# Performance work log

Measured on AMD Instinct MI355X. Metric: run time of the kernel, lower is better.

The kernel has to match this reference:

```python
import jax, jax.numpy as jnp
import numpy as np

B, T, D, H = 4, 2048, 1024, 16
HD = D // H  # head dim = 64


def setup_inputs() -> dict:
    key = jax.random.key(0)
    ks = jax.random.split(key, 12)
    s = 1.0 / np.sqrt(D)
    inp = {
        "Q": jax.random.normal(ks[0], (B, T, D), jnp.float32),
        "K": jax.random.normal(ks[1], (B, T, D), jnp.float32),
        "V": jax.random.normal(ks[2], (B, T, D), jnp.float32),
        "mask": jnp.tril(jnp.ones((T, T), jnp.int32))[None, None],  # causal [1,1,T,T]
        "Wq": jax.random.normal(ks[3], (D, D), jnp.float32) * s,
        "bq": jax.random.normal(ks[4], (D,), jnp.float32) * s,
        "Wk": jax.random.normal(ks[5], (D, D), jnp.float32) * s,
        "bk": jax.random.normal(ks[6], (D,), jnp.float32) * s,
        "Wv": jax.random.normal(ks[7], (D, D), jnp.float32) * s,
        "bv": jax.random.normal(ks[8], (D,), jnp.float32) * s,
        "Wo": jax.random.normal(ks[9], (D, D), jnp.float32) * s,
        "bo": jax.random.normal(ks[10], (D,), jnp.float32) * s,
    }
    return inp


def reference(Q, K, V, mask, Wq, bq, Wk, bk, Wv, bv, Wo, bo):
    b, t, d = Q.shape
    # projections (torch Linear: x @ W^T + b)
    q = (Q @ Wq.T + bq).reshape(b, t, H, HD).transpose(0, 2, 1, 3)  # [b,h,t,hd]
    k = (K @ Wk.T + bk).reshape(b, t, H, HD).transpose(0, 2, 1, 3)
    v = (V @ Wv.T + bv).reshape(b, t, H, HD).transpose(0, 2, 1, 3)
    score = jnp.einsum("bhqd,bhkd->bhqk", q, k) / jnp.sqrt(jnp.float32(HD))
    score = jnp.where(mask == 0, jnp.float32(-1e9), score)
    attn = jax.nn.softmax(score, axis=-1)
    out = jnp.einsum("bhqk,bhkd->bhqd", attn, v)
    out = out.transpose(0, 2, 1, 3).reshape(b, t, d)
    return out @ Wo.T + bo
```

## Files before the change

### kernel.cpp

```cpp
#include <hip/hip_runtime.h>
#include <stdint.h>

#define B_SZ  4
#define T_SEQ 2048
#define DIM   1024
#define NH    16
#define HD    64
#define M_TOT (B_SZ * T_SEQ)

typedef unsigned short u16;
typedef unsigned long long u64;
typedef __attribute__((ext_vector_type(8))) __bf16 bf16x8;
typedef __attribute__((ext_vector_type(4))) float  floatx4;
typedef __attribute__((ext_vector_type(16))) float floatx16;

#define SCL_Q (0.125f * 1.44269504089f)

__device__ __forceinline__ u16 f2bf(float f) {
  union { float f; uint32_t u; } v; v.f = f;
  uint32_t r = v.u + 0x7fffu + ((v.u >> 16) & 1u);
  return (u16)(r >> 16);
}

__device__ __forceinline__ void gl_lds16(const void* g, void* l) {
  __builtin_amdgcn_global_load_lds(
      (const __attribute__((address_space(1))) uint32_t*)g,
      (__attribute__((address_space(3))) uint32_t*)l, 16, 0, 0);
}

__global__ __launch_bounds__(256) void cvt_all(
    const float* __restrict__ s0, const float* __restrict__ s1,
    const float* __restrict__ s2, const float* __restrict__ s3,
    const float* __restrict__ s4, const float* __restrict__ s5,
    const float* __restrict__ s6,
    u16* __restrict__ d0, u16* __restrict__ d1, u16* __restrict__ d2,
    u16* __restrict__ d3, u16* __restrict__ d4, u16* __restrict__ d5,
    u16* __restrict__ d6) {
  const float* s; u16* d; int n;
  switch (blockIdx.y) {
    case 0: s = s0; d = d0; n = DIM * DIM; break;
    case 1: s = s1; d = d1; n = DIM * DIM; break;
    case 2: s = s2; d = d2; n = DIM * DIM; break;
    case 3: s = s3; d = d3; n = DIM * DIM; break;
    case 4: s = s4; d = d4; n = M_TOT * DIM; break;
    case 5: s = s5; d = d5; n = M_TOT * DIM; break;
    default: s = s6; d = d6; n = M_TOT * DIM; break;
  }
  int i = (blockIdx.x * 256 + threadIdx.x) * 8;
  if (i >= n) return;
  float4 a = *(const float4*)(s + i);
  float4 b = *(const float4*)(s + i + 4);
  uint4 o;
  o.x = (uint32_t)f2bf(a.x) | ((uint32_t)f2bf(a.y) << 16);
  o.y = (uint32_t)f2bf(a.z) | ((uint32_t)f2bf(a.w) << 16);
  o.z = (uint32_t)f2bf(b.x) | ((uint32_t)f2bf(b.y) << 16);
  o.w = (uint32_t)f2bf(b.z) | ((uint32_t)f2bf(b.w) << 16);
  *(uint4*)(d + i) = o;
}

#define BKG 64
__global__ __launch_bounds__(256) void gemm_qkv(
    const u16* __restrict__ Qb, const u16* __restrict__ Kb,
    const u16* __restrict__ Vb,
    const u16* __restrict__ Wq, const u16* __restrict__ Wk,
    const u16* __restrict__ Wv,
    const float* __restrict__ bq, const float* __restrict__ bk,
    const float* __restrict__ bv,
    u16* __restrict__ qo, u16* __restrict__ ko, u16* __restrict__ vo) {
  const u16* A; const u16* Bw; const float* bias; u16* Co;
  if (blockIdx.z == 0)      { A = Qb; Bw = Wq; bias = bq; Co = qo; }
  else if (blockIdx.z == 1) { A = Kb; Bw = Wk; bias = bk; Co = ko; }
  else                      { A = Vb; Bw = Wv; bias = bv; Co = vo; }

  __shared__ u16 As[128 * 64];
  __shared__ u16 Bs[128 * 64];

  const int tid  = threadIdx.x;
  const int wave = tid >> 6, lane = tid & 63;
  const int quad = lane >> 4, l16 = lane & 15;
  const int wm = wave >> 1, wn = wave & 1;
  const int m0 = blockIdx.x * 128, n0 = blockIdx.y * 128;

  const floatx4 FZ = {0.f, 0.f, 0.f, 0.f};
  floatx4 acc[4][4];
#pragma unroll
  for (int mt = 0; mt < 4; ++mt)
#pragma unroll
    for (int nt = 0; nt < 4; ++nt) acc[mt][nt] = FZ;

  for (int k0 = 0; k0 < DIM; k0 += BKG) {
    __syncthreads();
#pragma unroll
    for (int j = 0; j < 4; ++j) {
      int pc = j * 256 + tid;
      int r = pc >> 3, c = pc & 7;
      int sc = c ^ (r & 7);
      gl_lds16(A  + (size_t)(m0 + r) * DIM + k0 + sc * 8,
               &As[(j * 256 + wave * 64) * 8]);
      gl_lds16(Bw + (size_t)(n0 + r) * DIM + k0 + sc * 8,
               &Bs[(j * 256 + wave * 64) * 8]);
    }
    __syncthreads();

#pragma unroll
    for (int kk = 0; kk < 2; ++kk) {
      bf16x8 af[4], bfr[4];
#pragma unroll
      for (int mt = 0; mt < 4; ++mt) {
        int ra = wm * 64 + mt * 16 + l16;
        af[mt] = *(const bf16x8*)&As[ra * 64 + (((kk * 4 + quad) ^ (ra & 7)) * 8)];
      }
#pragma unroll
      for (int nt = 0; nt < 4; ++nt) {
        int rb = wn * 64 + nt * 16 + l16;
        bfr[nt] = *(const bf16x8*)&Bs[rb * 64 + (((kk * 4 + quad) ^ (rb & 7)) * 8)];
      }
#pragma unroll
      for (int mt = 0; mt < 4; ++mt)
#pragma unroll
        for (int nt = 0; nt < 4; ++nt)
          acc[mt][nt] = __builtin_amdgcn_mfma_f32_16x16x32_bf16(
              af[mt], bfr[nt], acc[mt][nt], 0, 0, 0);
    }
  }

  if (blockIdx.z == 2) {
#pragma unroll
    for (int nt = 0; nt < 4; ++nt) {
      int n = n0 + wn * 64 + nt * 16 + l16;
      float bb = bias[n];
      int h = n >> 6, hd = n & 63;
#pragma unroll
      for (int mt = 0; mt < 4; ++mt) {
        int mbase = m0 + wm * 64 + mt * 16 + quad * 4;
        int b = mbase >> 11, t = mbase & (T_SEQ - 1);
        u64 pk = 0;
#pragma unroll
        for (int r = 0; r < 4; ++r)
          pk |= (u64)f2bf(acc[mt][nt][r] + bb) << (16 * r);
        *(u64*)&Co[((size_t)((b * NH + h) * HD + hd)) * T_SEQ + t] = pk;
      }
    }
  } else {
    const float sc = (blockIdx.z == 0) ? SCL_Q : 1.0f;
#pragma unroll
    for (int nt = 0; nt < 4; ++nt) {
      int n = n0 + wn * 64 + nt * 16 + l16;
      float bb = bias[n];
      int h = n >> 6, hd = n & 63;
#pragma unroll
      for (int mt = 0; mt < 4; ++mt) {
#pragma unroll
        for (int r = 0; r < 4; ++r) {
          int m = m0 + wm * 64 + mt * 16 + quad * 4 + r;
          int b = m >> 11, t = m & (T_SEQ - 1);
          Co[((size_t)(b * NH + h) * T_SEQ + t) * HD + hd] =
              f2bf((acc[mt][nt][r] + bb) * sc);
        }
      }
    }
  }
}

__global__ __launch_bounds__(256, 2) void flash_attn(
    const u16* __restrict__ qp, const u16* __restrict__ kp,
    const u16* __restrict__ vp, u16* __restrict__ ao) {
  const int bh = blockIdx.x;
  const int y = blockIdx.y;
  const int qt = (y < 4) ? (7 - y) : (y - 4);
  const int b = bh >> 4, h = bh & 15;
  const u16* Qg = qp + (size_t)bh * T_SEQ * HD;
  const u16* Kg = kp + (size_t)bh * T_SEQ * HD;
  const u16* Vg = vp + (size_t)bh * HD * T_SEQ;

  __shared__ u16 lds[6][64 * 64];

  const int tid = threadIdx.x, wave = tid >> 6, lane = tid & 63;
  const int hi = lane >> 5, c31 = lane & 31;
  const int lr8 = lane >> 3, lc8 = lane & 7;

  const int wbase = qt * 256 + wave * 64;
  const int qrowA = wbase + c31;
  const int qrowB = qrowA + 32;

  bf16x8 bqA[4], bqB[4];
#pragma unroll
  for (int cth = 0; cth < 4; ++cth) {
    bqA[cth] = *(const bf16x8*)(Qg + (size_t)qrowA * HD + cth * 16 + hi * 8);
    bqB[cth] = *(const bf16x8*)(Qg + (size_t)qrowB * HD + cth * 16 + hi * 8);
  }

  const int nkb = 4 * qt + 4;

#define STAGE_KV(kbidx, bufpair)                                              \
  {                                                                           \
    const u16* Kgk = Kg + (size_t)(kbidx) * 64 * HD;                          \
    const u16* Vgk = Vg + (size_t)(kbidx) * 64;                               \
    _Pragma("unroll") for (int i_ = 0; i_ < 2; ++i_) {                        \
      int r_ = i_ * 32 + wave * 8 + lr8;                                      \
      int sc_ = lc8 ^ (r_ & 7);                                               \
      gl_lds16(Kgk + (size_t)r_ * HD + sc_ * 8,                               \
               &lds[(bufpair) * 2][(i_ * 32 + wave * 8) * 64]);               \
      gl_lds16(Vgk + (size_t)r_ * T_SEQ + sc_ * 8,                            \
               &lds[(bufpair) * 2 + 1][(i_ * 32 + wave * 8) * 64]);           \
    }                                                                         \
  }

  STAGE_KV(0, 0);
  STAGE_KV(1, 1);

  asm volatile("" :: "v"(bqA[0]), "v"(bqA[1]), "v"(bqA[2]), "v"(bqA[3]),
                     "v"(bqB[0]), "v"(bqB[1]), "v"(bqB[2]), "v"(bqB[3]));

  floatx16 oA0, oA1, oB0, oB1;
#pragma unroll
  for (int i = 0; i < 16; ++i) { oA0[i] = 0.f; oA1[i] = 0.f;
                                 oB0[i] = 0.f; oB1[i] = 0.f; }
  float l_pA = 0.f, l_pB = 0.f;

  int koff[4];
#pragma unroll
  for (int x = 0; x < 4; ++x)
    koff[x] = c31 * 64 + (((x * 2 + hi) ^ (c31 & 7)) * 8);

  int pcb = 0;
  int psb = 2;
  for (int kb = 0; kb < nkb; ++kb) {
    if (kb + 1 < nkb) asm volatile("s_waitcnt vmcnt(4)" ::: "memory");
    else              asm volatile("s_waitcnt vmcnt(0)" ::: "memory");
    __builtin_amdgcn_s_barrier();
    __builtin_amdgcn_sched_barrier(0);

    if (kb + 2 < nkb) {
      STAGE_KV(kb + 2, psb);
      psb = (psb == 2) ? 0 : psb + 1;
    }

    if (kb * 64 <= wbase + 63) {
      const u16* Ks = &lds[pcb * 2][0];
      const u16* Vs = &lds[pcb * 2 + 1][0];

      floatx16 sA0, sA1, sB0, sB1;
#pragma unroll
      for (int i = 0; i < 16; ++i) { sA0[i] = 0.f; sA1[i] = 0.f;
                                     sB0[i] = 0.f; sB1[i] = 0.f; }
#pragma unroll
      for (int cth = 0; cth < 4; ++cth) {
        bf16x8 ka = *(const bf16x8*)&Ks[koff[cth]];
        bf16x8 kh = *(const bf16x8*)&Ks[koff[cth] + 32 * 64];
        sA0 = __builtin_amdgcn_mfma_f32_32x32x16_bf16(ka, bqA[cth], sA0, 0, 0, 0);
        sA1 = __builtin_amdgcn_mfma_f32_32x32x16_bf16(kh, bqA[cth], sA1, 0, 0, 0);
        sB0 = __builtin_amdgcn_mfma_f32_32x32x16_bf16(ka, bqB[cth], sB0, 0, 0, 0);
        sB1 = __builtin_amdgcn_mfma_f32_32x32x16_bf16(kh, bqB[cth], sB1, 0, 0, 0);
      }

      if (kb * 64 + 63 > wbase) {
        int kvb = kb * 64 + 4 * hi;
#pragma unroll
        for (int r = 0; r < 16; ++r) {
          int kvr = kvb + (r & 3) + 8 * (r >> 2);
          if (kvr > qrowA)      sA0[r] = -3e38f;
          if (kvr + 32 > qrowA) sA1[r] = -3e38f;
          if (kvr > qrowB)      sB0[r] = -3e38f;
          if (kvr + 32 > qrowB) sB1[r] = -3e38f;
        }
      }

      uint32_t pkA0[8], pkA1[8], pkB0[8], pkB1[8];
      float rsA = 0.f, rsB = 0.f;
#pragma unroll
      for (int rr = 0; rr < 8; ++rr) {
        union { float f; uint32_t u; } x0, x1, y0, y1;
        x0.f = __builtin_amdgcn_exp2f(sA0[2 * rr]);
        x1.f = __builtin_amdgcn_exp2f(sA0[2 * rr + 1]);
        y0.f = __builtin_amdgcn_exp2f(sA1[2 * rr]);
        y1.f = __builtin_amdgcn_exp2f(sA1[2 * rr + 1]);
        rsA += (x0.f + x1.f) + (y0.f + y1.f);
        pkA0[rr] = __builtin_amdgcn_perm(x1.u, x0.u, 0x07060302);
        pkA1[rr] = __builtin_amdgcn_perm(y1.u, y0.u, 0x07060302);
        x0.f = __builtin_amdgcn_exp2f(sB0[2 * rr]);
        x1.f = __builtin_amdgcn_exp2f(sB0[2 * rr + 1]);
        y0.f = __builtin_amdgcn_exp2f(sB1[2 * rr]);
        y1.f = __builtin_amdgcn_exp2f(sB1[2 * rr + 1]);
        rsB += (x0.f + x1.f) + (y0.f + y1.f);
        pkB0[rr] = __builtin_amdgcn_perm(x1.u, x0.u, 0x07060302);
        pkB1[rr] = __builtin_amdgcn_perm(y1.u, y0.u, 0x07060302);
      }
      l_pA += rsA;
      l_pB += rsB;

#pragma unroll
      for (int cc = 0; cc < 4; ++cc) {
        const uint32_t* pA = (cc & 2) ? pkA1 : pkA0;
        const uint32_t* pB = (cc & 2) ? pkB1 : pkB0;
        const int e4 = (cc & 1) * 4;
        auto a0 = __builtin_amdgcn_permlane32_swap(pA[e4 + 0], pA[e4 + 2],
                                                   false, false);
        auto a1 = __builtin_amdgcn_permlane32_swap(pA[e4 + 1], pA[e4 + 3],
                                                   false, false);
        auto b0 = __builtin_amdgcn_permlane32_swap(pB[e4 + 0], pB[e4 + 2],
                                                   false, false);
        auto b1 = __builtin_amdgcn_permlane32_swap(pB[e4 + 1], pB[e4 + 3],
                                                   false, false);
        union { uint32_t u[4]; bf16x8 v; } bpA, bpB;
        bpA.u[0] = a0[0]; bpA.u[1] = a1[0]; bpA.u[2] = a0[1]; bpA.u[3] = a1[1];
        bpB.u[0] = b0[0]; bpB.u[1] = b1[0]; bpB.u[2] = b0[1]; bpB.u[3] = b1[1];
        bf16x8 va = *(const bf16x8*)&Vs[koff[cc]];
        bf16x8 vb = *(const bf16x8*)&Vs[koff[cc] + 32 * 64];
        oA0 = __builtin_amdgcn_mfma_f32_32x32x16_bf16(va, bpA.v, oA0, 0, 0, 0);
        oA1 = __builtin_amdgcn_mfma_f32_32x32x16_bf16(vb, bpA.v, oA1, 0, 0, 0);
        oB0 = __builtin_amdgcn_mfma_f32_32x32x16_bf16(va, bpB.v, oB0, 0, 0, 0);
        oB1 = __builtin_amdgcn_mfma_f32_32x32x16_bf16(vb, bpB.v, oB1, 0, 0, 0);
      }
    }
    pcb = (pcb == 2) ? 0 : pcb + 1;
  }
#undef STAGE_KV

  {
    float lA = l_pA + __shfl_xor(l_pA, 32);
    float lB = l_pB + __shfl_xor(l_pB, 32);
    float invA = 1.0f / lA, invB = 1.0f / lB;
    const size_t obaseA = (size_t)(b * T_SEQ + qrowA) * DIM + h * HD;
    const size_t obaseB = obaseA + (size_t)32 * DIM;
#pragma unroll
    for (int u4 = 0; u4 < 4; ++u4) {
      u64 wA0 = 0, wA1 = 0, wB0 = 0, wB1 = 0;
#pragma unroll
      for (int r = 0; r < 4; ++r) {
        wA0 |= (u64)f2bf(oA0[4 * u4 + r] * invA) << (16 * r);
        wA1 |= (u64)f2bf(oA1[4 * u4 + r] * invA) << (16 * r);
        wB0 |= (u64)f2bf(oB0[4 * u4 + r] * invB) << (16 * r);
        wB1 |= (u64)f2bf(oB1[4 * u4 + r] * invB) << (16 * r);
      }
      *(u64*)&ao[obaseA + 8 * u4 + 4 * hi] = wA0;
      *(u64*)&ao[obaseA + 32 + 8 * u4 + 4 * hi] = wA1;
      *(u64*)&ao[obaseB + 8 * u4 + 4 * hi] = wB0;
      *(u64*)&ao[obaseB + 32 + 8 * u4 + 4 * hi] = wB1;
    }
  }
}

__global__ __launch_bounds__(256) void gemm_out(
    const u16* __restrict__ Ain, const u16* __restrict__ Wo,
    const float* __restrict__ bo, float* __restrict__ out) {
  __shared__ u16 As[128 * 64];
  __shared__ u16 Bs[128 * 64];

  const int tid  = threadIdx.x;
  const int wave = tid >> 6, lane = tid & 63;
  const int quad = lane >> 4, l16 = lane & 15;
  const int wm = wave >> 1, wn = wave & 1;
  const int m0 = blockIdx.x * 128, n0 = blockIdx.y * 128;

  const floatx4 FZ = {0.f, 0.f, 0.f, 0.f};
  floatx4 acc[4][4];
#pragma unroll
  for (int mt = 0; mt < 4; ++mt)
#pragma unroll
    for (int nt = 0; nt < 4; ++nt) acc[mt][nt] = FZ;

  for (int k0 = 0; k0 < DIM; k0 += BKG) {
    __syncthreads();
#pragma unroll
    for (int j = 0; j < 4; ++j) {
      int pc = j * 256 + tid;
      int r = pc >> 3, c = pc & 7;
      int sc = c ^ (r & 7);
      gl_lds16(Ain + (size_t)(m0 + r) * DIM + k0 + sc * 8,
               &As[(j * 256 + wave * 64) * 8]);
      gl_lds16(Wo  + (size_t)(n0 + r) * DIM + k0 + sc * 8,
               &Bs[(j * 256 + wave * 64) * 8]);
    }
    __syncthreads();

#pragma unroll
    for (int kk = 0; kk < 2; ++kk) {
      bf16x8 af[4], bfr[4];
#pragma unroll
      for (int mt = 0; mt < 4; ++mt) {
        int ra = wm * 64 + mt * 16 + l16;
        af[mt] = *(const bf16x8*)&As[ra * 64 + (((kk * 4 + quad) ^ (ra & 7)) * 8)];
      }
#pragma unroll
      for (int nt = 0; nt < 4; ++nt) {
        int rb = wn * 64 + nt * 16 + l16;
        bfr[nt] = *(const bf16x8*)&Bs[rb * 64 + (((kk * 4 + quad) ^ (rb & 7)) * 8)];
      }
#pragma unroll
      for (int mt = 0; mt < 4; ++mt)
#pragma unroll
        for (int nt = 0; nt < 4; ++nt)
          acc[mt][nt] = __builtin_amdgcn_mfma_f32_16x16x32_bf16(
              af[mt], bfr[nt], acc[mt][nt], 0, 0, 0);
    }
  }

#pragma unroll
  for (int nt = 0; nt < 4; ++nt) {
    int n = n0 + wn * 64 + nt * 16 + l16;
    float bb = bo[n];
#pragma unroll
    for (int mt = 0; mt < 4; ++mt)
#pragma unroll
      for (int r = 0; r < 4; ++r) {
        int m = m0 + wm * 64 + mt * 16 + quad * 4 + r;
        out[(size_t)m * DIM + n] = acc[mt][nt][r] + bb;
      }
  }
}

extern "C" void kernel_launch(void* const* d_in, const int* in_sizes, int n_in,
                              void* d_out, int out_size, void* d_ws,
                              size_t ws_size, hipStream_t stream) {
  const float* Q  = (const float*)d_in[0];
  const float* K  = (const float*)d_in[1];
  const float* V  = (const float*)d_in[2];
  const float* Wq = (const float*)d_in[4];
  const float* bq = (const float*)d_in[5];
  const float* Wk = (const float*)d_in[6];
  const float* bk = (const float*)d_in[7];
  const float* Wv = (const float*)d_in[8];
  const float* bv = (const float*)d_in[9];
  const float* Wo = (const float*)d_in[10];
  const float* bo = (const float*)d_in[11];
  float* out = (float*)d_out;

  u16* wqb = (u16*)d_ws;
  u16* wkb = wqb + 1048576;
  u16* wvb = wkb + 1048576;
  u16* wob = wvb + 1048576;
  u16* Qb  = wob + 1048576;
  u16* Kb  = Qb + (size_t)M_TOT * DIM;
  u16* Vb  = Kb + (size_t)M_TOT * DIM;
  u16* qp  = Vb + (size_t)M_TOT * DIM;
  u16* kp  = qp + (size_t)M_TOT * DIM;
  u16* vp  = kp + (size_t)M_TOT * DIM;
  u16* aop = vp + (size_t)M_TOT * DIM;

  cvt_all<<<dim3(M_TOT * DIM / 2048, 7), 256, 0, stream>>>(
      Wq, Wk, Wv, Wo, Q, K, V, wqb, wkb, wvb, wob, Qb, Kb, Vb);

  gemm_qkv<<<dim3(M_TOT / 128, DIM / 128, 3), 256, 0, stream>>>(
      Qb, Kb, Vb, wqb, wkb, wvb, bq, bk, bv, qp, kp, vp);

  flash_attn<<<dim3(B_SZ * NH, T_SEQ / 256), 256, 0, stream>>>(qp, kp, vp, aop);

  gemm_out<<<dim3(M_TOT / 128, DIM / 128), 256, 0, stream>>>(aop, wob, bo, out);
}
```

Measured before the change: 308.2 us.

## Fuse fp32-to-bf16 activation conversion into QKV GEMM and double-buffer weights

Drops the separate conversion pass over the Q/K/V activations. The QKV GEMM now reads fp32 rows straight from global memory into registers and converts them to bf16 just before the MFMA, so the bf16 activation copies no longer have to be written and read back. The weight tile is double-buffered in LDS with async global-to-LDS loads for the next k-step. The cost is that each block re-reads A rows from global memory as fp32, at twice the bytes, across the 8 column blocks of the grid, with no LDS sharing. These loads are per-lane 16-byte reads with a stride of one row, which may coalesce poorly.

New measurement: 427.0 us. 38.6% more time.

```diff
diff --git a/kernel.cpp b/kernel.cpp
--- a/kernel.cpp
+++ b/kernel.cpp
@@ -28,26 +28,19 @@
       (__attribute__((address_space(3))) uint32_t*)l, 16, 0, 0);
 }
 
-__global__ __launch_bounds__(256) void cvt_all(
+__global__ __launch_bounds__(256) void cvt_w(
     const float* __restrict__ s0, const float* __restrict__ s1,
     const float* __restrict__ s2, const float* __restrict__ s3,
-    const float* __restrict__ s4, const float* __restrict__ s5,
-    const float* __restrict__ s6,
     u16* __restrict__ d0, u16* __restrict__ d1, u16* __restrict__ d2,
-    u16* __restrict__ d3, u16* __restrict__ d4, u16* __restrict__ d5,
-    u16* __restrict__ d6) {
-  const float* s; u16* d; int n;
+    u16* __restrict__ d3) {
+  const float* s; u16* d;
   switch (blockIdx.y) {
-    case 0: s = s0; d = d0; n = DIM * DIM; break;
-    case 1: s = s1; d = d1; n = DIM * DIM; break;
-    case 2: s = s2; d = d2; n = DIM * DIM; break;
-    case 3: s = s3; d = d3; n = DIM * DIM; break;
-    case 4: s = s4; d = d4; n = M_TOT * DIM; break;
-    case 5: s = s5; d = d5; n = M_TOT * DIM; break;
-    default: s = s6; d = d6; n = M_TOT * DIM; break;
+    case 0: s = s0; d = d0; break;
+    case 1: s = s1; d = d1; break;
+    case 2: s = s2; d = d2; break;
+    default: s = s3; d = d3; break;
   }
   int i = (blockIdx.x * 256 + threadIdx.x) * 8;
-  if (i >= n) return;
   float4 a = *(const float4*)(s + i);
   float4 b = *(const float4*)(s + i + 4);
   uint4 o;
@@ -58,22 +51,22 @@
   *(uint4*)(d + i) = o;
 }
 
-#define BKG 64
+#define BKG  64
+#define NT_K (DIM / BKG)
 __global__ __launch_bounds__(256) void gemm_qkv(
-    const u16* __restrict__ Qb, const u16* __restrict__ Kb,
-    const u16* __restrict__ Vb,
+    const float* __restrict__ Qf, const float* __restrict__ Kf,
+    const float* __restrict__ Vf,
     const u16* __restrict__ Wq, const u16* __restrict__ Wk,
     const u16* __restrict__ Wv,
     const float* __restrict__ bq, const float* __restrict__ bk,
     const float* __restrict__ bv,
     u16* __restrict__ qo, u16* __restrict__ ko, u16* __restrict__ vo) {
-  const u16* A; const u16* Bw; const float* bias; u16* Co;
-  if (blockIdx.z == 0)      { A = Qb; Bw = Wq; bias = bq; Co = qo; }
-  else if (blockIdx.z == 1) { A = Kb; Bw = Wk; bias = bk; Co = ko; }
-  else                      { A = Vb; Bw = Wv; bias = bv; Co = vo; }
-
-  __shared__ u16 As[128 * 64];
-  __shared__ u16 Bs[128 * 64];
+  const float* A; const u16* Bw; const float* bias; u16* Co;
+  if (blockIdx.z == 0)      { A = Qf; Bw = Wq; bias = bq; Co = qo; }
+  else if (blockIdx.z == 1) { A = Kf; Bw = Wk; bias = bk; Co = ko; }
+  else                      { A = Vf; Bw = Wv; bias = bv; Co = vo; }
+
+  __shared__ u16 Bs[2][128 * 64];
 
   const int tid  = threadIdx.x;
   const int wave = tid >> 6, lane = tid & 63;
@@ -88,41 +81,66 @@
 #pragma unroll
     for (int nt = 0; nt < 4; ++nt) acc[mt][nt] = FZ;
 
-  for (int k0 = 0; k0 < DIM; k0 += BKG) {
-    __syncthreads();
-#pragma unroll
-    for (int j = 0; j < 4; ++j) {
-      int pc = j * 256 + tid;
-      int r = pc >> 3, c = pc & 7;
-      int sc = c ^ (r & 7);
-      gl_lds16(A  + (size_t)(m0 + r) * DIM + k0 + sc * 8,
-               &As[(j * 256 + wave * 64) * 8]);
-      gl_lds16(Bw + (size_t)(n0 + r) * DIM + k0 + sc * 8,
-               &Bs[(j * 256 + wave * 64) * 8]);
-    }
-    __syncthreads();
+  const float* arow0 = A + (size_t)(m0 + wm * 64 + 0 * 16 + l16) * DIM + quad * 8;
+  const float* arow1 = A + (size_t)(m0 + wm * 64 + 1 * 16 + l16) * DIM + quad * 8;
+  const float* arow2 = A + (size_t)(m0 + wm * 64 + 2 * 16 + l16) * DIM + quad * 8;
+  const float* arow3 = A + (size_t)(m0 + wm * 64 + 3 * 16 + l16) * DIM + quad * 8;
+
+#define STAGE_B(kt)                                                           \
+  { _Pragma("unroll") for (int j_ = 0; j_ < 4; ++j_) {                        \
+      int pc_ = j_ * 256 + tid; int r_ = pc_ >> 3, c_ = pc_ & 7;              \
+      int sc_ = c_ ^ (r_ & 7);                                                \
+      gl_lds16(Bw + (size_t)(n0 + r_) * DIM + (kt) * BKG + sc_ * 8,           \
+               &Bs[(kt) & 1][(j_ * 256 + wave * 64) * 8]); } }
+
+  STAGE_B(0);
+  __syncthreads();
+
+  for (int t = 0; t < NT_K; ++t) {
+    const int k0 = t * BKG;
+
+    float4 a4[4][2][2];
+#pragma unroll
+    for (int kk = 0; kk < 2; ++kk)
+#pragma unroll
+      for (int h = 0; h < 2; ++h) {
+        a4[0][kk][h] = *(const float4*)(arow0 + k0 + kk * 32 + h * 4);
+        a4[1][kk][h] = *(const float4*)(arow1 + k0 + kk * 32 + h * 4);
+        a4[2][kk][h] = *(const float4*)(arow2 + k0 + kk * 32 + h * 4);
+        a4[3][kk][h] = *(const float4*)(arow3 + k0 + kk * 32 + h * 4);
+      }
+
+    if (t + 1 < NT_K) STAGE_B(t + 1);
+
+    bf16x8 bfr[4][2];
+#pragma unroll
+    for (int nt = 0; nt < 4; ++nt) {
+      int rb = wn * 64 + nt * 16 + l16;
+#pragma unroll
+      for (int kk = 0; kk < 2; ++kk)
+        bfr[nt][kk] = *(const bf16x8*)
+            &Bs[t & 1][rb * 64 + (((kk * 4 + quad) ^ (rb & 7)) * 8)];
+    }
 
 #pragma unroll
     for (int kk = 0; kk < 2; ++kk) {
-      bf16x8 af[4], bfr[4];
 #pragma unroll
       for (int mt = 0; mt < 4; ++mt) {
-        int ra = wm * 64 + mt * 16 + l16;
-        af[mt] = *(const bf16x8*)&As[ra * 64 + (((kk * 4 + quad) ^ (ra & 7)) * 8)];
-      }
-#pragma unroll
-      for (int nt = 0; nt < 4; ++nt) {
-        int rb = wn * 64 + nt * 16 + l16;
-        bfr[nt] = *(const bf16x8*)&Bs[rb * 64 + (((kk * 4 + quad) ^ (rb & 7)) * 8)];
-      }
-#pragma unroll
-      for (int mt = 0; mt < 4; ++mt)
+        float4 lo = a4[mt][kk][0], hi = a4[mt][kk][1];
+        bf16x8 af;
+        af[0] = (__bf16)lo.x; af[1] = (__bf16)lo.y;
+        af[2] = (__bf16)lo.z; af[3] = (__bf16)lo.w;
+        af[4] = (__bf16)hi.x; af[5] = (__bf16)hi.y;
+        af[6] = (__bf16)hi.z; af[7] = (__bf16)hi.w;
 #pragma unroll
         for (int nt = 0; nt < 4; ++nt)
           acc[mt][nt] = __builtin_amdgcn_mfma_f32_16x16x32_bf16(
-              af[mt], bfr[nt], acc[mt][nt], 0, 0, 0);
-    }
-  }
+              af, bfr[nt][kk], acc[mt][nt], 0, 0, 0);
+      }
+    }
+    __syncthreads();
+  }
+#undef STAGE_B
 
   if (blockIdx.z == 2) {
 #pragma unroll
@@ -430,19 +448,16 @@
   u16* wkb = wqb + 1048576;
   u16* wvb = wkb + 1048576;
   u16* wob = wvb + 1048576;
-  u16* Qb  = wob + 1048576;
-  u16* Kb  = Qb + (size_t)M_TOT * DIM;
-  u16* Vb  = Kb + (size_t)M_TOT * DIM;
-  u16* qp  = Vb + (size_t)M_TOT * DIM;
+  u16* qp  = wob + 1048576;
   u16* kp  = qp + (size_t)M_TOT * DIM;
   u16* vp  = kp + (size_t)M_TOT * DIM;
   u16* aop = vp + (size_t)M_TOT * DIM;
 
-  cvt_all<<<dim3(M_TOT * DIM / 2048, 7), 256, 0, stream>>>(
-      Wq, Wk, Wv, Wo, Q, K, V, wqb, wkb, wvb, wob, Qb, Kb, Vb);
+  cvt_w<<<dim3(DIM * DIM / 2048, 4), 256, 0, stream>>>(
+      Wq, Wk, Wv, Wo, wqb, wkb, wvb, wob);
 
   gemm_qkv<<<dim3(M_TOT / 128, DIM / 128, 3), 256, 0, stream>>>(
-      Qb, Kb, Vb, wqb, wkb, wvb, bq, bk, bv, qp, kp, vp);
+      Q, K, V, wqb, wkb, wvb, bq, bk, bv, qp, kp, vp);
 
   flash_attn<<<dim3(B_SZ * NH, T_SEQ / 256), 256, 0, stream>>>(qp, kp, vp, aop);
 
```

## Triple-buffer QKV projection GEMM with async global-to-LDS prefetch

Applied to the files above, without the earlier changes.

Reworks the QKV projection GEMM main loop into a three-stage LDS ring buffer with K-tile 32. Loads for tile t+2 are issued before computing tile t, and each iteration uses a single barrier guarded by explicit vmcnt waits instead of two syncthreads. The goal is to hide global load latency behind MFMA work. The cost is more loop iterations with less compute each, a new XOR swizzle for 32-wide rows, and hand-managed waitcnt correctness. The output-projection GEMM keeps a hardcoded K step of 64.

Measured after the change: 318.3 us. 1.03x slower.

```diff
diff --git a/kernel.cpp b/kernel.cpp
--- a/kernel.cpp
+++ b/kernel.cpp
@@ -58,7 +58,8 @@
   *(uint4*)(d + i) = o;
 }
 
-#define BKG 64
+#define BKG  32
+#define NT_K (DIM / BKG)
 __global__ __launch_bounds__(256) void gemm_qkv(
     const u16* __restrict__ Qb, const u16* __restrict__ Kb,
     const u16* __restrict__ Vb,
@@ -72,12 +73,13 @@
   else if (blockIdx.z == 1) { A = Kb; Bw = Wk; bias = bk; Co = ko; }
   else                      { A = Vb; Bw = Wv; bias = bv; Co = vo; }
 
-  __shared__ u16 As[128 * 64];
-  __shared__ u16 Bs[128 * 64];
+  __shared__ u16 As[3][128 * 32];
+  __shared__ u16 Bs[3][128 * 32];
 
   const int tid  = threadIdx.x;
   const int wave = tid >> 6, lane = tid & 63;
   const int quad = lane >> 4, l16 = lane & 15;
+  const int lr4 = lane >> 2, lc4 = lane & 3;
   const int wm = wave >> 1, wn = wave & 1;
   const int m0 = blockIdx.x * 128, n0 = blockIdx.y * 128;
 
@@ -88,41 +90,55 @@
 #pragma unroll
     for (int nt = 0; nt < 4; ++nt) acc[mt][nt] = FZ;
 
-  for (int k0 = 0; k0 < DIM; k0 += BKG) {
-    __syncthreads();
-#pragma unroll
-    for (int j = 0; j < 4; ++j) {
-      int pc = j * 256 + tid;
-      int r = pc >> 3, c = pc & 7;
-      int sc = c ^ (r & 7);
-      gl_lds16(A  + (size_t)(m0 + r) * DIM + k0 + sc * 8,
-               &As[(j * 256 + wave * 64) * 8]);
-      gl_lds16(Bw + (size_t)(n0 + r) * DIM + k0 + sc * 8,
-               &Bs[(j * 256 + wave * 64) * 8]);
-    }
-    __syncthreads();
-
-#pragma unroll
-    for (int kk = 0; kk < 2; ++kk) {
-      bf16x8 af[4], bfr[4];
-#pragma unroll
-      for (int mt = 0; mt < 4; ++mt) {
-        int ra = wm * 64 + mt * 16 + l16;
-        af[mt] = *(const bf16x8*)&As[ra * 64 + (((kk * 4 + quad) ^ (ra & 7)) * 8)];
-      }
-#pragma unroll
-      for (int nt = 0; nt < 4; ++nt) {
-        int rb = wn * 64 + nt * 16 + l16;
-        bfr[nt] = *(const bf16x8*)&Bs[rb * 64 + (((kk * 4 + quad) ^ (rb & 7)) * 8)];
-      }
-#pragma unroll
-      for (int mt = 0; mt < 4; ++mt)
-#pragma unroll
-        for (int nt = 0; nt < 4; ++nt)
-          acc[mt][nt] = __builtin_amdgcn_mfma_f32_16x16x32_bf16(
-              af[mt], bfr[nt], acc[mt][nt], 0, 0, 0);
-    }
-  }
+#define STAGE_AB(kt, buf)                                                     \
+  { _Pragma("unroll") for (int i_ = 0; i_ < 2; ++i_) {                        \
+      int rb_ = wave * 32 + i_ * 16;                                          \
+      int r_ = rb_ + lr4;                                                     \
+      int sc_ = lc4 ^ ((r_ >> 1) & 3);                                        \
+      gl_lds16(A  + (size_t)(m0 + r_) * DIM + (kt) * BKG + sc_ * 8,           \
+               &As[buf][rb_ * 32]);                                           \
+      gl_lds16(Bw + (size_t)(n0 + r_) * DIM + (kt) * BKG + sc_ * 8,           \
+               &Bs[buf][rb_ * 32]);                                           \
+    } }
+
+  STAGE_AB(0, 0);
+  STAGE_AB(1, 1);
+
+  int rd = 0, st = 2;
+  for (int t = 0; t < NT_K; ++t) {
+    if (t + 1 < NT_K) asm volatile("s_waitcnt vmcnt(4)" ::: "memory");
+    else              asm volatile("s_waitcnt vmcnt(0)" ::: "memory");
+    __builtin_amdgcn_s_barrier();
+    __builtin_amdgcn_sched_barrier(0);
+
+    if (t + 2 < NT_K) {
+      STAGE_AB(t + 2, st);
+      st = (st == 2) ? 0 : st + 1;
+    }
+
+    bf16x8 af[4], bfr[4];
+#pragma unroll
+    for (int mt = 0; mt < 4; ++mt) {
+      int ra = wm * 64 + mt * 16 + l16;
+      af[mt] = *(const bf16x8*)
+          &As[rd][ra * 32 + ((quad ^ ((ra >> 1) & 3)) * 8)];
+    }
+#pragma unroll
+    for (int nt = 0; nt < 4; ++nt) {
+      int rb = wn * 64 + nt * 16 + l16;
+      bfr[nt] = *(const bf16x8*)
+          &Bs[rd][rb * 32 + ((quad ^ ((rb >> 1) & 3)) * 8)];
+    }
+#pragma unroll
+    for (int mt = 0; mt < 4; ++mt)
+#pragma unroll
+      for (int nt = 0; nt < 4; ++nt)
+        acc[mt][nt] = __builtin_amdgcn_mfma_f32_16x16x32_bf16(
+            af[mt], bfr[nt], acc[mt][nt], 0, 0, 0);
+
+    rd = (rd == 2) ? 0 : rd + 1;
+  }
+#undef STAGE_AB
 
   if (blockIdx.z == 2) {
 #pragma unroll
@@ -133,12 +149,12 @@
 #pragma unroll
       for (int mt = 0; mt < 4; ++mt) {
         int mbase = m0 + wm * 64 + mt * 16 + quad * 4;
-        int b = mbase >> 11, t = mbase & (T_SEQ - 1);
+        int b = mbase >> 11, tq = mbase & (T_SEQ - 1);
         u64 pk = 0;
 #pragma unroll
         for (int r = 0; r < 4; ++r)
           pk |= (u64)f2bf(acc[mt][nt][r] + bb) << (16 * r);
-        *(u64*)&Co[((size_t)((b * NH + h) * HD + hd)) * T_SEQ + t] = pk;
+        *(u64*)&Co[((size_t)((b * NH + h) * HD + hd)) * T_SEQ + tq] = pk;
       }
     }
   } else {
@@ -153,8 +169,8 @@
 #pragma unroll
         for (int r = 0; r < 4; ++r) {
           int m = m0 + wm * 64 + mt * 16 + quad * 4 + r;
-          int b = m >> 11, t = m & (T_SEQ - 1);
-          Co[((size_t)(b * NH + h) * T_SEQ + t) * HD + hd] =
+          int b = m >> 11, tq = m & (T_SEQ - 1);
+          Co[((size_t)(b * NH + h) * T_SEQ + tq) * HD + hd] =
               f2bf((acc[mt][nt][r] + bb) * sc);
         }
       }
@@ -360,7 +376,7 @@
 #pragma unroll
     for (int nt = 0; nt < 4; ++nt) acc[mt][nt] = FZ;
 
-  for (int k0 = 0; k0 < DIM; k0 += BKG) {
+  for (int k0 = 0; k0 < DIM; k0 += 64) {
     __syncthreads();
 #pragma unroll
     for (int j = 0; j < 4; ++j) {
```

## Fuse fp32-to-bf16 activation conversion into the QKV projection GEMM

Applied to the files above, without the earlier changes.

The separate conversion of Q, K and V activations to bf16 is removed. The QKV GEMM now streams fp32 activation tiles straight into LDS and converts them to bf16 while building MFMA fragments. This drops a full read and write pass over three 8M-element tensors and their workspace buffers. In exchange the GEMM reads twice as many bytes for A, and the larger LDS footprint (32KB for A) may lower occupancy. The conversion switches from explicit round-to-nearest-even to the compiler's __bf16 cast.

Result: slower. 401.2 us (+30.2%).

```diff
diff --git a/kernel.cpp b/kernel.cpp
--- a/kernel.cpp
+++ b/kernel.cpp
@@ -28,26 +28,19 @@
       (__attribute__((address_space(3))) uint32_t*)l, 16, 0, 0);
 }
 
-__global__ __launch_bounds__(256) void cvt_all(
+__global__ __launch_bounds__(256) void cvt_w(
     const float* __restrict__ s0, const float* __restrict__ s1,
     const float* __restrict__ s2, const float* __restrict__ s3,
-    const float* __restrict__ s4, const float* __restrict__ s5,
-    const float* __restrict__ s6,
     u16* __restrict__ d0, u16* __restrict__ d1, u16* __restrict__ d2,
-    u16* __restrict__ d3, u16* __restrict__ d4, u16* __restrict__ d5,
-    u16* __restrict__ d6) {
-  const float* s; u16* d; int n;
+    u16* __restrict__ d3) {
+  const float* s; u16* d;
   switch (blockIdx.y) {
-    case 0: s = s0; d = d0; n = DIM * DIM; break;
-    case 1: s = s1; d = d1; n = DIM * DIM; break;
-    case 2: s = s2; d = d2; n = DIM * DIM; break;
-    case 3: s = s3; d = d3; n = DIM * DIM; break;
-    case 4: s = s4; d = d4; n = M_TOT * DIM; break;
-    case 5: s = s5; d = d5; n = M_TOT * DIM; break;
-    default: s = s6; d = d6; n = M_TOT * DIM; break;
+    case 0: s = s0; d = d0; break;
+    case 1: s = s1; d = d1; break;
+    case 2: s = s2; d = d2; break;
+    default: s = s3; d = d3; break;
   }
   int i = (blockIdx.x * 256 + threadIdx.x) * 8;
-  if (i >= n) return;
   float4 a = *(const float4*)(s + i);
   float4 b = *(const float4*)(s + i + 4);
   uint4 o;
@@ -60,20 +53,20 @@
 
 #define BKG 64
 __global__ __launch_bounds__(256) void gemm_qkv(
-    const u16* __restrict__ Qb, const u16* __restrict__ Kb,
-    const u16* __restrict__ Vb,
+    const float* __restrict__ Qf, const float* __restrict__ Kf,
+    const float* __restrict__ Vf,
     const u16* __restrict__ Wq, const u16* __restrict__ Wk,
     const u16* __restrict__ Wv,
     const float* __restrict__ bq, const float* __restrict__ bk,
     const float* __restrict__ bv,
     u16* __restrict__ qo, u16* __restrict__ ko, u16* __restrict__ vo) {
-  const u16* A; const u16* Bw; const float* bias; u16* Co;
-  if (blockIdx.z == 0)      { A = Qb; Bw = Wq; bias = bq; Co = qo; }
-  else if (blockIdx.z == 1) { A = Kb; Bw = Wk; bias = bk; Co = ko; }
-  else                      { A = Vb; Bw = Wv; bias = bv; Co = vo; }
-
-  __shared__ u16 As[128 * 64];
-  __shared__ u16 Bs[128 * 64];
+  const float* Af; const u16* Bw; const float* bias; u16* Co;
+  if (blockIdx.z == 0)      { Af = Qf; Bw = Wq; bias = bq; Co = qo; }
+  else if (blockIdx.z == 1) { Af = Kf; Bw = Wk; bias = bk; Co = ko; }
+  else                      { Af = Vf; Bw = Wv; bias = bv; Co = vo; }
+
+  __shared__ float Asf[128 * 64];
+  __shared__ u16   Bs[128 * 64];
 
   const int tid  = threadIdx.x;
   const int wave = tid >> 6, lane = tid & 63;
@@ -91,12 +84,18 @@
   for (int k0 = 0; k0 < DIM; k0 += BKG) {
     __syncthreads();
 #pragma unroll
+    for (int j = 0; j < 8; ++j) {
+      int pc = j * 256 + tid;
+      int r = pc >> 4, c = pc & 15;
+      int sc = c ^ ((r & 7) << 1);
+      gl_lds16(Af + (size_t)(m0 + r) * DIM + k0 + sc * 4,
+               &Asf[(size_t)(j * 16 + wave * 4) * 64]);
+    }
+#pragma unroll
     for (int j = 0; j < 4; ++j) {
       int pc = j * 256 + tid;
       int r = pc >> 3, c = pc & 7;
       int sc = c ^ (r & 7);
-      gl_lds16(A  + (size_t)(m0 + r) * DIM + k0 + sc * 8,
-               &As[(j * 256 + wave * 64) * 8]);
       gl_lds16(Bw + (size_t)(n0 + r) * DIM + k0 + sc * 8,
                &Bs[(j * 256 + wave * 64) * 8]);
     }
@@ -108,7 +107,16 @@
 #pragma unroll
       for (int mt = 0; mt < 4; ++mt) {
         int ra = wm * 64 + mt * 16 + l16;
-        af[mt] = *(const bf16x8*)&As[ra * 64 + (((kk * 4 + quad) ^ (ra & 7)) * 8)];
+        int c0 = (quad * 2 + kk * 8) ^ ((ra & 7) << 1);
+        const float* ap = &Asf[(size_t)ra * 64 + c0 * 4];
+        float4 lo = *(const float4*)ap;
+        float4 hi = *(const float4*)(ap + 4);
+        bf16x8 a;
+        a[0] = (__bf16)lo.x; a[1] = (__bf16)lo.y;
+        a[2] = (__bf16)lo.z; a[3] = (__bf16)lo.w;
+        a[4] = (__bf16)hi.x; a[5] = (__bf16)hi.y;
+        a[6] = (__bf16)hi.z; a[7] = (__bf16)hi.w;
+        af[mt] = a;
       }
 #pragma unroll
       for (int nt = 0; nt < 4; ++nt) {
@@ -430,19 +438,16 @@
   u16* wkb = wqb + 1048576;
   u16* wvb = wkb + 1048576;
   u16* wob = wvb + 1048576;
-  u16* Qb  = wob + 1048576;
-  u16* Kb  = Qb + (size_t)M_TOT * DIM;
-  u16* Vb  = Kb + (size_t)M_TOT * DIM;
-  u16* qp  = Vb + (size_t)M_TOT * DIM;
+  u16* qp  = wob + 1048576;
   u16* kp  = qp + (size_t)M_TOT * DIM;
   u16* vp  = kp + (size_t)M_TOT * DIM;
   u16* aop = vp + (size_t)M_TOT * DIM;
 
-  cvt_all<<<dim3(M_TOT * DIM / 2048, 7), 256, 0, stream>>>(
-      Wq, Wk, Wv, Wo, Q, K, V, wqb, wkb, wvb, wob, Qb, Kb, Vb);
+  cvt_w<<<dim3(DIM * DIM / 2048, 4), 256, 0, stream>>>(
+      Wq, Wk, Wv, Wo, wqb, wkb, wvb, wob);
 
   gemm_qkv<<<dim3(M_TOT / 128, DIM / 128, 3), 256, 0, stream>>>(
-      Qb, Kb, Vb, wqb, wkb, wvb, bq, bk, bv, qp, kp, vp);
+      Q, K, V, wqb, wkb, wvb, bq, bk, bv, qp, kp, vp);
 
   flash_attn<<<dim3(B_SZ * NH, T_SEQ / 256), 256, 0, stream>>>(qp, kp, vp, aop);
 
```
